# Performance work log

Measured on AMD Instinct MI355X. Metric: run time of the kernel, lower is better.

Reference implementation:

```python
import jax, jax.numpy as jnp
import numpy as np

B, H, L, D = 4, 16, 2048, 128


def setup_inputs() -> dict:
    key = jax.random.key(0)
    kx, kw1, kb1, kw2, kb2 = jax.random.split(key, 5)
    s = 1.0 / np.sqrt(D)
    return {
        "x": jax.random.normal(kx, (B, H, L, D), dtype=jnp.float32),
        "W1": jax.random.uniform(kw1, (D, D), jnp.float32, -s, s),
        "b1": jax.random.uniform(kb1, (D,), jnp.float32, -s, s),
        "W2": jax.random.uniform(kw2, (D, D), jnp.float32, -s, s),
        "b2": jax.random.uniform(kb2, (D,), jnp.float32, -s, s),
    }


def reference(x, W1, b1, W2, b2):
    # proj_1/proj_2: Linear(dim, dim) on the last axis (torch stores W as [out,in])
    q = jnp.einsum('bhld,ed->bhle', x, W1) + b1  # [B,H,L,D]
    k = jnp.einsum('bhld,ed->bhle', x, W2) + b2  # [B,H,L,D]
    # exact-erf GELU on raw QK^T scores, then softmax over j
    adj = jax.nn.gelu(jnp.einsum('bhid,bhjd->bhij', q, k), approximate=False)
    adj = jax.nn.softmax(adj, axis=-1)  # [B,H,L,L]
    # dropout is identity in eval mode
    out = jnp.einsum('bhij,bhjd->bhid', adj, x)  # [B,H,L,D]
    return out.transpose(0, 2, 1, 3).reshape(B, L, H * D)
```

## Files before the change

### kernel.cpp

```cpp
#include <hip/hip_runtime.h>
#include <hip/hip_bf16.h>

#define B_ 4
#define H_ 16
#define L_ 2048
#define D_ 128
#define BH_ 64

typedef __attribute__((ext_vector_type(8))) _Float16 f16x8;
typedef __attribute__((ext_vector_type(4))) float f32x4;
typedef __attribute__((ext_vector_type(16))) float f32x16;
typedef __attribute__((ext_vector_type(2))) unsigned u32x2;

#define L2E 1.44269504088896f

__device__ __forceinline__ float gelu_l2e(float v) {
  float x  = v * 0.70710678118f;
  float ax = __builtin_fabsf(x);
  float t  = __builtin_amdgcn_rcpf(__builtin_fmaf(0.3275911f, ax, 1.0f));
  float poly = t * __builtin_fmaf(t,
                 __builtin_fmaf(t,
                   __builtin_fmaf(t,
                     __builtin_fmaf(t, 1.061405429f, -1.453152027f),
                   1.421413741f),
                 -0.284496736f),
               0.254829592f);
  float e    = __builtin_amdgcn_exp2f(-L2E * x * x);
  float erfa = __builtin_fmaf(-poly, e, 1.0f);
  float erfx = copysignf(erfa, x);
  float hv   = 0.72134752f * v;
  return __builtin_fmaf(hv, erfx, hv);
}

__device__ __forceinline__ void gl2lds16(const void* g, void* l) {
  __builtin_amdgcn_global_load_lds(
      (const __attribute__((address_space(1))) void*)g,
      (__attribute__((address_space(3))) void*)l, 16, 0, 0);
}

__device__ __forceinline__ unsigned pkrtz(float a, float b) {
  auto t = __builtin_amdgcn_cvt_pkrtz(a, b);
  return __builtin_bit_cast(unsigned, t);
}

__global__ __launch_bounds__(256) void wcvt_kernel(
    const float* __restrict__ W1, const float* __restrict__ W2,
    _Float16* __restrict__ Wh1, _Float16* __restrict__ Wh2)
{
  int i = blockIdx.x * 256 + threadIdx.x;
  Wh1[i] = (_Float16)W1[i];
  Wh2[i] = (_Float16)W2[i];
}

__global__ __launch_bounds__(256) void proj_tr_kernel(
    const float* __restrict__ x,
    const _Float16* __restrict__ Wh1, const float* __restrict__ b1,
    const _Float16* __restrict__ Wh2, const float* __restrict__ b2,
    _Float16* __restrict__ Qb, _Float16* __restrict__ Kb,
    _Float16* __restrict__ VT)
{
  const int tid  = threadIdx.x;
  const int wave = tid >> 6;
  const int lane = tid & 63;
  const int lhi  = lane >> 4;
  const int llo  = lane & 15;
  const int r0   = blockIdx.x * 64;
  const int wr0  = r0 + wave * 16;

  f16x8 a[4];
#pragma unroll
  for (int ks = 0; ks < 4; ++ks) {
    const float* p = x + (size_t)(wr0 + llo) * D_ + lhi * 8 + ks * 32;
    f16x8 t;
#pragma unroll
    for (int e = 0; e < 8; ++e) t[e] = (_Float16)p[e];
    a[ks] = t;
  }

  f32x4 accq[8], acck[8];
#pragma unroll
  for (int n = 0; n < 8; ++n) {
    accq[n] = (f32x4){0.f, 0.f, 0.f, 0.f};
    acck[n] = (f32x4){0.f, 0.f, 0.f, 0.f};
  }

#pragma unroll
  for (int n = 0; n < 8; ++n) {
    const int e = n * 16 + llo;
#pragma unroll
    for (int ks = 0; ks < 4; ++ks) {
      f16x8 w1f = *(const f16x8*)(Wh1 + (size_t)e * D_ + lhi * 8 + ks * 32);
      f16x8 w2f = *(const f16x8*)(Wh2 + (size_t)e * D_ + lhi * 8 + ks * 32);
      accq[n] = __builtin_amdgcn_mfma_f32_16x16x32_f16(a[ks], w1f, accq[n], 0, 0, 0);
      acck[n] = __builtin_amdgcn_mfma_f32_16x16x32_f16(a[ks], w2f, acck[n], 0, 0, 0);
    }
  }

#pragma unroll
  for (int n = 0; n < 8; ++n) {
    const int e = n * 16 + llo;
    const float bias1 = b1[e];
    const float bias2 = b2[e];
#pragma unroll
    for (int r = 0; r < 4; ++r) {
      const size_t row = (size_t)wr0 + lhi * 4 + r;
      Qb[row * D_ + e] = (_Float16)(accq[n][r] + bias1);
      Kb[row * D_ + e] = (_Float16)(acck[n][r] + bias2);
    }
  }

  const int bh = r0 / L_;
  const int l0 = r0 % L_;
  const int d  = tid & 127;
  const int rh = tid >> 7;
  _Float16* dst = VT + (size_t)bh * D_ * L_ + (size_t)d * L_ + l0 + rh * 32;
#pragma unroll
  for (int j = 0; j < 4; ++j) {
    f16x8 t;
#pragma unroll
    for (int e = 0; e < 8; ++e)
      t[e] = (_Float16)x[(size_t)(r0 + rh * 32 + j * 8 + e) * D_ + d];
    *(f16x8*)(dst + j * 8) = t;
  }
}

__global__ __launch_bounds__(512) void attn_kernel(
    const _Float16* __restrict__ Qb, const _Float16* __restrict__ Kb,
    const _Float16* __restrict__ VT, float* __restrict__ out)
{
  __shared__ _Float16 Ks[2][64 * 128];
  __shared__ _Float16 Vs[2][128 * 64];

  const int tid  = threadIdx.x;
  const int wave = tid >> 6;
  const int lane = tid & 63;
  const int l5   = lane & 31;
  const int hi   = lane >> 5;

  const int bid = blockIdx.x;
  const int blk = (bid & 7) * 64 + (bid >> 3);
  const int bh  = blk >> 3;
  const int q0  = (blk & 7) * 256;
  const int b   = bh >> 4;
  const int h   = bh & 15;
  const int wq0 = q0 + wave * 32;

  const char* KheadB = (const char*)(Kb + (size_t)bh * L_ * D_);
  const char* VheadB = (const char*)(VT + (size_t)bh * D_ * L_);

  int klds[2], ksrc[2], vlds[2], vsrc[2];
#pragma unroll
  for (int c = 0; c < 2; ++c) {
    const int wc = wave * 2 + c;
    klds[c] = wc * 1024;
    {
      const int l  = wc * 4 + (lane >> 4);
      const int c0 = (lane & 15) * 8;
      ksrc[c] = l * 256 + 2 * (c0 ^ ((l & 7) << 3));
    }
    vlds[c] = wc * 1024;
    {
      const int d  = wc * 8 + (lane >> 3);
      const int c0 = (lane & 7) * 8;
      vsrc[c] = d * 4096 + 2 * (c0 ^ ((d & 7) << 3));
    }
  }
  const int kvswz = (l5 & 7) << 3;

  f16x8 qf[8];
#pragma unroll
  for (int s = 0; s < 8; ++s)
    qf[s] = *(const f16x8*)(Qb + ((size_t)bh * L_ + wq0 + l5) * D_ + s * 16 + hi * 8);

  f32x16 accO[4];
#pragma unroll
  for (int n = 0; n < 4; ++n)
#pragma unroll
    for (int r = 0; r < 16; ++r) accO[n][r] = 0.f;
  float m = -1e30f;
  float l = 0.f;

#pragma unroll
  for (int c = 0; c < 2; ++c) {
    gl2lds16(KheadB + ksrc[c], (char*)&Ks[0][0] + klds[c]);
    gl2lds16(VheadB + vsrc[c], (char*)&Vs[0][0] + vlds[c]);
  }
  __syncthreads();

  int cur = 0;
  for (int t = 0; t < L_ / 64; ++t) {
    if (t + 1 < L_ / 64) {
      const char* kt_ = KheadB + (size_t)(t + 1) * 64 * 256;
      const char* vt_ = VheadB + (size_t)(t + 1) * 128;
#pragma unroll
      for (int c = 0; c < 2; ++c) {
        gl2lds16(kt_ + ksrc[c], (char*)&Ks[cur ^ 1][0] + klds[c]);
        gl2lds16(vt_ + vsrc[c], (char*)&Vs[cur ^ 1][0] + vlds[c]);
      }
    }
    const _Float16* Kcur = &Ks[cur][0];
    const _Float16* Vcur = &Vs[cur][0];

#pragma unroll
    for (int kb = 0; kb < 2; ++kb) {
      f32x16 sT;
#pragma unroll
      for (int r = 0; r < 16; ++r) sT[r] = 0.f;
      __builtin_amdgcn_s_setprio(1);
#pragma unroll
      for (int s = 0; s < 8; ++s) {
        f16x8 kf = *(const f16x8*)(Kcur + (kb * 32 + l5) * 128 +
                                   ((s * 16 + hi * 8) ^ kvswz));
        sT = __builtin_amdgcn_mfma_f32_32x32x16_f16(kf, qf[s], sT, 0, 0, 0);
      }
      __builtin_amdgcn_s_setprio(0);

      float g[16];
#pragma unroll
      for (int r = 0; r < 16; ++r) g[r] = gelu_l2e(sT[r]);

      float tm = fmaxf(g[0], g[1]);
#pragma unroll
      for (int r = 2; r < 16; ++r) tm = fmaxf(tm, g[r]);
      tm = fmaxf(tm, __shfl_xor(tm, 32));

      float p[16];
      float ts = 0.f;
      if (__all(tm <= m + 11.5415603f)) {
#pragma unroll
        for (int r = 0; r < 16; ++r) {
          p[r] = __builtin_amdgcn_exp2f(g[r] - m);
          ts += p[r];
        }
        ts += __shfl_xor(ts, 32);
        l += ts;
      } else {
        float mn = fmaxf(m, tm);
        float sc = __builtin_amdgcn_exp2f(m - mn);
        m = mn;
#pragma unroll
        for (int r = 0; r < 16; ++r) {
          p[r] = __builtin_amdgcn_exp2f(g[r] - m);
          ts += p[r];
        }
        ts += __shfl_xor(ts, 32);
        l = __builtin_fmaf(l, sc, ts);
        float scr[16];
#pragma unroll
        for (int r = 0; r < 16; ++r)
          scr[r] = __shfl(sc, (r & 3) + 8 * (r >> 2) + 4 * hi);
#pragma unroll
        for (int n = 0; n < 4; ++n)
#pragma unroll
          for (int r = 0; r < 16; ++r) accO[n][r] *= scr[r];
      }

      unsigned pk01 = pkrtz(p[0], p[1]),   pk23 = pkrtz(p[2], p[3]);
      unsigned pk45 = pkrtz(p[4], p[5]),   pk67 = pkrtz(p[6], p[7]);
      unsigned pk89 = pkrtz(p[8], p[9]),   pkAB = pkrtz(p[10], p[11]);
      unsigned pkCD = pkrtz(p[12], p[13]), pkEF = pkrtz(p[14], p[15]);
      u32x2 r0 = __builtin_amdgcn_permlane32_swap(pk01, pk45, false, false);
      u32x2 r1 = __builtin_amdgcn_permlane32_swap(pk23, pk67, false, false);
      u32x2 r2 = __builtin_amdgcn_permlane32_swap(pk89, pkCD, false, false);
      u32x2 r3 = __builtin_amdgcn_permlane32_swap(pkAB, pkEF, false, false);
      union { unsigned u[4]; f16x8 v; } A0c, A1c;
      A0c.u[0] = r0[0]; A0c.u[1] = r1[0]; A0c.u[2] = r0[1]; A0c.u[3] = r1[1];
      A1c.u[0] = r2[0]; A1c.u[1] = r3[0]; A1c.u[2] = r2[1]; A1c.u[3] = r3[1];

      __builtin_amdgcn_s_setprio(1);
#pragma unroll
      for (int n = 0; n < 4; ++n) {
        f16x8 vf0 = *(const f16x8*)(Vcur + (n * 32 + l5) * 64 +
                                    ((kb * 32 + hi * 8) ^ kvswz));
        accO[n] = __builtin_amdgcn_mfma_f32_32x32x16_f16(A0c.v, vf0, accO[n], 0, 0, 0);
        f16x8 vf1 = *(const f16x8*)(Vcur + (n * 32 + l5) * 64 +
                                    ((kb * 32 + 16 + hi * 8) ^ kvswz));
        accO[n] = __builtin_amdgcn_mfma_f32_32x32x16_f16(A1c.v, vf1, accO[n], 0, 0, 0);
      }
      __builtin_amdgcn_s_setprio(0);
    }

    __syncthreads();
    cur ^= 1;
  }

  float linv = __builtin_amdgcn_rcpf(l);
  float lb[16];
#pragma unroll
  for (int r = 0; r < 16; ++r)
    lb[r] = __shfl(linv, (r & 3) + 8 * (r >> 2) + 4 * hi);
#pragma unroll
  for (int n = 0; n < 4; ++n)
#pragma unroll
    for (int r = 0; r < 16; ++r) {
      const int i = wq0 + (r & 3) + 8 * (r >> 2) + 4 * hi;
      out[((size_t)(b * L_ + i) * H_ + h) * D_ + n * 32 + l5] = accO[n][r] * lb[r];
    }
}

extern "C" void kernel_launch(void* const* d_in, const int* in_sizes, int n_in,
                              void* d_out, int out_size, void* d_ws, size_t ws_size,
                              hipStream_t stream) {
  const float* x  = (const float*)d_in[0];
  const float* W1 = (const float*)d_in[1];
  const float* b1 = (const float*)d_in[2];
  const float* W2 = (const float*)d_in[3];
  const float* b2 = (const float*)d_in[4];
  float* out = (float*)d_out;

  const size_t N = (size_t)BH_ * L_ * D_;
  _Float16* Qb = (_Float16*)d_ws;
  _Float16* Kb = Qb + N;
  _Float16* VT = Kb + N;

  _Float16* Wh1 = (_Float16*)d_out;
  _Float16* Wh2 = Wh1 + D_ * D_;

  wcvt_kernel<<<64, 256, 0, stream>>>(W1, W2, Wh1, Wh2);
  proj_tr_kernel<<<(BH_ * L_) / 64, 256, 0, stream>>>(x, Wh1, b1, Wh2, b2, Qb, Kb, VT);
  attn_kernel<<<BH_ * (L_ / 256), 512, 0, stream>>>(Qb, Kb, VT, out);
}
```

Before: 394.5 us.

## Fold running-max subtraction into GELU and tree-reduce softmax sums

The GELU is rewritten so the running max offset is folded into its final FMA, and it returns log2-scaled score minus max directly. This removes the per-element subtraction before exp2 and some multiplies. The running max is tracked as a negated offset starting at an initial value, so the skip-rescale test compares against a constant. The change also adds tree reductions for the row sum and max, unrolls the tile loop by 2 with a derived buffer index, and sets a launch-bounds occupancy hint, which risks register pressure.

Result: slower. 1.492 ms (+278.2%).

```diff
diff --git a/kernel.cpp b/kernel.cpp
--- a/kernel.cpp
+++ b/kernel.cpp
@@ -14,10 +14,10 @@
 
 #define L2E 1.44269504088896f
 
-__device__ __forceinline__ float gelu_l2e(float v) {
-  float x  = v * 0.70710678118f;
-  float ax = __builtin_fabsf(x);
-  float t  = __builtin_amdgcn_rcpf(__builtin_fmaf(0.3275911f, ax, 1.0f));
+__device__ __forceinline__ float gelu_m(float v, float negm) {
+  float x    = v * 0.70710678118f;
+  float ax   = __builtin_fabsf(x);
+  float t    = __builtin_amdgcn_rcpf(__builtin_fmaf(0.3275911f, ax, 1.0f));
   float poly = t * __builtin_fmaf(t,
                  __builtin_fmaf(t,
                    __builtin_fmaf(t,
@@ -25,11 +25,12 @@
                    1.421413741f),
                  -0.284496736f),
                0.254829592f);
-  float e    = __builtin_amdgcn_exp2f(-L2E * x * x);
-  float erfa = __builtin_fmaf(-poly, e, 1.0f);
-  float erfx = copysignf(erfa, x);
-  float hv   = 0.72134752f * v;
-  return __builtin_fmaf(hv, erfx, hv);
+  float nv   = -0.72134752f * v;
+  float e    = __builtin_amdgcn_exp2f(nv * v);
+  float hva  = __builtin_fabsf(nv);
+  float relm = fmaxf(__builtin_fmaf(1.44269504f, v, negm), negm);
+  float pe   = poly * e;
+  return __builtin_fmaf(hva, -pe, relm);
 }
 
 __device__ __forceinline__ void gl2lds16(const void* g, void* l) {
@@ -124,7 +125,7 @@
   }
 }
 
-__global__ __launch_bounds__(512) void attn_kernel(
+__global__ __launch_bounds__(512, 4) void attn_kernel(
     const _Float16* __restrict__ Qb, const _Float16* __restrict__ Kb,
     const _Float16* __restrict__ VT, float* __restrict__ out)
 {
@@ -177,7 +178,7 @@
   for (int n = 0; n < 4; ++n)
 #pragma unroll
     for (int r = 0; r < 16; ++r) accO[n][r] = 0.f;
-  float m = -1e30f;
+  float negm = 64.f;
   float l = 0.f;
 
 #pragma unroll
@@ -187,8 +188,9 @@
   }
   __syncthreads();
 
-  int cur = 0;
+#pragma unroll 2
   for (int t = 0; t < L_ / 64; ++t) {
+    const int cur = t & 1;
     if (t + 1 < L_ / 64) {
       const char* kt_ = KheadB + (size_t)(t + 1) * 64 * 256;
       const char* vt_ = VheadB + (size_t)(t + 1) * 128;
@@ -215,34 +217,39 @@
       }
       __builtin_amdgcn_s_setprio(0);
 
-      float g[16];
-#pragma unroll
-      for (int r = 0; r < 16; ++r) g[r] = gelu_l2e(sT[r]);
-
-      float tm = fmaxf(g[0], g[1]);
-#pragma unroll
-      for (int r = 2; r < 16; ++r) tm = fmaxf(tm, g[r]);
+      float gm[16];
+#pragma unroll
+      for (int r = 0; r < 16; ++r) gm[r] = gelu_m(sT[r], negm);
+
+      float tm = fmaxf(fmaxf(gm[0], gm[1]), gm[2]);
+      tm = fmaxf(fmaxf(tm, gm[3]),  gm[4]);
+      tm = fmaxf(fmaxf(tm, gm[5]),  gm[6]);
+      tm = fmaxf(fmaxf(tm, gm[7]),  gm[8]);
+      tm = fmaxf(fmaxf(tm, gm[9]),  gm[10]);
+      tm = fmaxf(fmaxf(tm, gm[11]), gm[12]);
+      tm = fmaxf(fmaxf(tm, gm[13]), gm[14]);
+      tm = fmaxf(tm, gm[15]);
       tm = fmaxf(tm, __shfl_xor(tm, 32));
 
       float p[16];
-      float ts = 0.f;
-      if (__all(tm <= m + 11.5415603f)) {
-#pragma unroll
-        for (int r = 0; r < 16; ++r) {
-          p[r] = __builtin_amdgcn_exp2f(g[r] - m);
-          ts += p[r];
-        }
+      float ts;
+      if (__all(tm <= 11.5415603f)) {
+#pragma unroll
+        for (int r = 0; r < 16; ++r) p[r] = __builtin_amdgcn_exp2f(gm[r]);
+        float a0 = p[0]+p[1],   a1 = p[2]+p[3],   a2 = p[4]+p[5],   a3 = p[6]+p[7];
+        float a4 = p[8]+p[9],   a5 = p[10]+p[11], a6 = p[12]+p[13], a7 = p[14]+p[15];
+        ts = ((a0+a1)+(a2+a3)) + ((a4+a5)+(a6+a7));
         ts += __shfl_xor(ts, 32);
         l += ts;
       } else {
-        float mn = fmaxf(m, tm);
-        float sc = __builtin_amdgcn_exp2f(m - mn);
-        m = mn;
-#pragma unroll
-        for (int r = 0; r < 16; ++r) {
-          p[r] = __builtin_amdgcn_exp2f(g[r] - m);
-          ts += p[r];
-        }
+        float dm = fmaxf(tm, 0.f);
+        negm -= dm;
+        float sc = __builtin_amdgcn_exp2f(-dm);
+#pragma unroll
+        for (int r = 0; r < 16; ++r) p[r] = __builtin_amdgcn_exp2f(gm[r] - dm);
+        float a0 = p[0]+p[1],   a1 = p[2]+p[3],   a2 = p[4]+p[5],   a3 = p[6]+p[7];
+        float a4 = p[8]+p[9],   a5 = p[10]+p[11], a6 = p[12]+p[13], a7 = p[14]+p[15];
+        ts = ((a0+a1)+(a2+a3)) + ((a4+a5)+(a6+a7));
         ts += __shfl_xor(ts, 32);
         l = __builtin_fmaf(l, sc, ts);
         float scr[16];
@@ -281,7 +288,6 @@
     }
 
     __syncthreads();
-    cur ^= 1;
   }
 
   float linv = __builtin_amdgcn_rcpf(l);
```
